# Performance work log

Measured on AMD Instinct MI355X. Metric: run time of the kernel, lower is better.

Reference implementation:

```python
import jax, jax.numpy as jnp
import numpy as np

C = 512
QK = C // 8  # 64
B, L = 8, 4096


def setup_inputs() -> dict:
    key = jax.random.key(0)
    ks = jax.random.split(key, 8)
    s = 0.02
    return {
        "x": jax.random.normal(ks[0], (B, C, L), dtype=jnp.float32),
        "Wq": jax.random.normal(ks[1], (QK, C), dtype=jnp.float32) * s,
        "bq": jax.random.normal(ks[2], (QK,), dtype=jnp.float32) * s,
        "Wk": jax.random.normal(ks[3], (QK, C), dtype=jnp.float32) * s,
        "bk": jax.random.normal(ks[4], (QK,), dtype=jnp.float32) * s,
        "Wv": jax.random.normal(ks[5], (C, C), dtype=jnp.float32) * s,
        "bv": jax.random.normal(ks[6], (C,), dtype=jnp.float32) * s,
        "gamma": jax.random.normal(ks[7], (1,), dtype=jnp.float32) * 0.1,
    }


def reference(x, Wq, bq, Wk, bk, Wv, bv, gamma):
    # 1x1 convs are per-position linear projections over channels
    q = jnp.einsum('bcl,dc->bld', x, Wq) + bq            # [B, L, QK]  (proj_query, permuted)
    k = jnp.einsum('bcl,dc->bdl', x, Wk) + bk[:, None]   # [B, QK, L]  (proj_key)
    v = jnp.einsum('bcl,dc->bdl', x, Wv) + bv[:, None]   # [B, C, L]   (proj_value)
    energy = jnp.einsum('bid,bdj->bij', q, k)            # [B, L, L]
    attn = jax.nn.softmax(energy, axis=-1)               # softmax over j
    out = jnp.einsum('bcj,bij->bci', v, attn)            # [B, C, L]
    return gamma * out + x
```

## Files before the change

kernel.cpp:

```cpp
#include <hip/hip_runtime.h>
#include <math.h>

#define BB 8
#define CC 512
#define LL 4096
#define DQK 64

typedef short short8 __attribute__((ext_vector_type(8)));
typedef unsigned short ushort4v __attribute__((ext_vector_type(4)));
typedef unsigned short ushort8v __attribute__((ext_vector_type(8)));
typedef float floatx4 __attribute__((ext_vector_type(4)));
typedef unsigned int uint4v __attribute__((ext_vector_type(4)));

__device__ __forceinline__ unsigned short f2bf(float f) {
    union { float f; unsigned u; } v; v.f = f;
    unsigned r = v.u + 0x7fffu + ((v.u >> 16) & 1u);
    return (unsigned short)(r >> 16);
}

__device__ __forceinline__ void load_lds16(const void* gptr, void* lptr) {
    __builtin_amdgcn_global_load_lds(
        (const __attribute__((address_space(1))) unsigned int*)gptr,
        (__attribute__((address_space(3))) unsigned int*)lptr, 16, 0, 0);
}

__device__ __forceinline__ unsigned cvt_pk_bf16(float lo, float hi) {
    unsigned r;
    asm("v_cvt_pk_bf16_f32 %0, %1, %2" : "=v"(r) : "v"(lo), "v"(hi));
    return r;
}

__global__ __launch_bounds__(256) void k_transpose(const float* __restrict__ x,
                                                   unsigned short* __restrict__ xt) {
    __shared__ unsigned short tile[64][72];
    int l0 = blockIdx.x * 64, c0 = blockIdx.y * 64, b = blockIdx.z;
    int t = threadIdx.x;
    int r  = t >> 2;
    int ch = (t & 3) * 16;
    const float* src = x + ((size_t)b * CC + c0 + r) * LL + l0 + ch;
#pragma unroll
    for (int j = 0; j < 4; ++j) {
        floatx4 v = *(const floatx4*)(src + j * 4);
        ushort4v u = { f2bf(v[0]), f2bf(v[1]), f2bf(v[2]), f2bf(v[3]) };
        *(ushort4v*)(&tile[r][ch + j * 4]) = u;
    }
    __syncthreads();
    int lr  = t >> 2;
    int cch = (t & 3) * 16;
    ushort8v o0, o1;
#pragma unroll
    for (int j = 0; j < 8; ++j) o0[j] = tile[cch + j][lr];
#pragma unroll
    for (int j = 0; j < 8; ++j) o1[j] = tile[cch + 8 + j][lr];
    unsigned short* dst = xt + ((size_t)b * LL + l0 + lr) * CC + c0 + cch;
    *(ushort8v*)(dst)     = o0;
    *(ushort8v*)(dst + 8) = o1;
}

__global__ void k_castw(const float* __restrict__ wq, const float* __restrict__ wk,
                        const float* __restrict__ wv,
                        unsigned short* __restrict__ wqb, unsigned short* __restrict__ wkb,
                        unsigned short* __restrict__ wvb) {
    int i = blockIdx.x * 256 + threadIdx.x;
    if (i < DQK * CC) { wqb[i] = f2bf(wq[i]); wkb[i] = f2bf(wk[i]); }
    wvb[i] = f2bf(wv[i]);
}

__global__ __launch_bounds__(256) void k_proj(const unsigned short* __restrict__ xt,
                                              const unsigned short* __restrict__ wb,
                                              const float* __restrict__ bias,
                                              unsigned short* __restrict__ out,
                                              float scale) {
    int l0 = blockIdx.x * 64;
    int b  = blockIdx.y;
    int tid = threadIdx.x;
    int w = tid >> 6, lane = tid & 63;
    int lane16 = lane & 15, g = lane >> 4;
    __shared__ unsigned short wtile[64 * 512];
    {
        int pg = tid & 63;
#pragma unroll
        for (int ci = 0; ci < 16; ++ci) {
            int r  = ci * 4 + (tid >> 6);
            int sg = (pg & 56) | ((pg ^ r) & 7);
            load_lds16(wb + (size_t)r * CC + sg * 8, wtile + ((size_t)ci * 256 + tid) * 8);
        }
    }
    const unsigned short* xrow = xt + ((size_t)b * LL + l0 + w * 16 + lane16) * CC + g * 8;
    short8 afrag[16];
#pragma unroll
    for (int kk = 0; kk < 16; ++kk) afrag[kk] = *(const short8*)(xrow + kk * 32);
    __syncthreads();

    int xe = (g ^ (lane16 & 7)) * 8;
    int xo = ((g + 4) ^ (lane16 & 7)) * 8;
#pragma unroll
    for (int nt = 0; nt < 4; ++nt) {
        int dl = nt * 16 + lane16;
        floatx4 acc = {0.f, 0.f, 0.f, 0.f};
#pragma unroll
        for (int kk = 0; kk < 16; ++kk) {
            int off = dl * 512 + (kk >> 1) * 64 + ((kk & 1) ? xo : xe);
            short8 bfrag = *(const short8*)(wtile + off);
            acc = __builtin_amdgcn_mfma_f32_16x16x32_bf16(afrag[kk], bfrag, acc, 0, 0, 0);
        }
        float bv = bias[dl];
#pragma unroll
        for (int r = 0; r < 4; ++r) {
            int lidx = l0 + w * 16 + g * 4 + r;
            out[((size_t)b * LL + lidx) * DQK + dl] = f2bf((acc[r] + bv) * scale);
        }
    }
}

__global__ __launch_bounds__(256) void k_projT(const unsigned short* __restrict__ xt,
                                               const unsigned short* __restrict__ wb,
                                               const float* __restrict__ bias,
                                               unsigned short* __restrict__ out) {
    int l0 = blockIdx.x * 64;
    int b  = blockIdx.y;
    int tid = threadIdx.x;
    int w = tid >> 6, lane = tid & 63;
    int lane16 = lane & 15, g = lane >> 4;
    __shared__ unsigned short xtile[64 * 512];
    {
        const unsigned short* xg = xt + ((size_t)b * LL + l0) * CC;
        int pg = tid & 63;
#pragma unroll
        for (int ci = 0; ci < 16; ++ci) {
            int r  = ci * 4 + (tid >> 6);
            int sg = (pg & 56) | ((pg ^ r) & 7);
            load_lds16(xg + (size_t)r * CC + sg * 8, xtile + ((size_t)ci * 256 + tid) * 8);
        }
    }
    __syncthreads();

    int xe = (g ^ (lane16 & 7)) * 8;
    int xo = ((g + 4) ^ (lane16 & 7)) * 8;
    for (int z = 0; z < 8; ++z) {
        int dw = z * 64 + w * 16;
        const unsigned short* wrow = wb + (size_t)(dw + lane16) * CC + g * 8;
        short8 afrag[16];
#pragma unroll
        for (int kk = 0; kk < 16; ++kk) afrag[kk] = *(const short8*)(wrow + kk * 32);
#pragma unroll
        for (int nt = 0; nt < 4; ++nt) {
            floatx4 acc = {0.f, 0.f, 0.f, 0.f};
#pragma unroll
            for (int kk = 0; kk < 16; ++kk) {
                int off = (nt * 16 + lane16) * 512 + (kk >> 1) * 64 + ((kk & 1) ? xo : xe);
                short8 bfrag = *(const short8*)(xtile + off);
                acc = __builtin_amdgcn_mfma_f32_16x16x32_bf16(afrag[kk], bfrag, acc, 0, 0, 0);
            }
            int l = l0 + nt * 16 + lane16;
#pragma unroll
            for (int r = 0; r < 4; ++r) {
                int d = dw + g * 4 + r;
                out[((size_t)b * CC + d) * LL + l] = f2bf(acc[r] + bias[d]);
            }
        }
    }
}

__global__ __launch_bounds__(256, 2) void k_attn(const unsigned short* __restrict__ q,
                                                 const unsigned short* __restrict__ kws,
                                                 const unsigned short* __restrict__ vws,
                                                 const float* __restrict__ x,
                                                 const float* __restrict__ gamma,
                                                 float* __restrict__ out) {
    int i0 = blockIdx.x * 128;
    int b  = blockIdx.y;
    int c0 = blockIdx.z * 256;
    int tid = threadIdx.x;
    int w = tid >> 6, lane = tid & 63;
    int lane16 = lane & 15, g = lane >> 4;
    int iw = i0 + w * 32;

    __shared__ unsigned short kt[2][64 * 64];
    __shared__ unsigned short vt[2][256 * 64];

    short8 qf[2][2];
#pragma unroll
    for (int m = 0; m < 2; ++m) {
        const unsigned short* qrow = q + ((size_t)b * LL + iw + m * 16 + lane16) * DQK + g * 8;
        qf[m][0] = *(const short8*)(qrow);
        qf[m][1] = *(const short8*)(qrow + 32);
    }

    const unsigned short* kglob = kws + (size_t)b * LL * DQK;
    const unsigned short* vglob = vws + ((size_t)b * CC + c0) * LL;
    int gr    = (tid & 7) ^ ((tid >> 3) & 7);
    int koff0 = (tid >> 3) * DQK + gr * 8;
    int voff0 = (tid >> 3) * LL  + gr * 8;

    int kro[2], vro[2];
#pragma unroll
    for (int kk = 0; kk < 2; ++kk) {
        int sw = (kk * 4 + g) ^ (lane16 & 7);
        kro[kk] = lane16 * 64 + sw * 8;
        vro[kk] = lane16 * 64 + sw * 8;
    }

    short8 ones;
#pragma unroll
    for (int j = 0; j < 8; ++j) ones[j] = (short)0x3f80;

    floatx4 O[2][16];
#pragma unroll
    for (int m = 0; m < 2; ++m)
#pragma unroll
        for (int nt = 0; nt < 16; ++nt) O[m][nt] = {0.f, 0.f, 0.f, 0.f};
    floatx4 Ol[2];
#pragma unroll
    for (int m = 0; m < 2; ++m) Ol[m] = {0.f, 0.f, 0.f, 0.f};

    auto stage = [&](int j0n, int buf) {
        const unsigned short* ks = kglob + j0n * DQK + koff0;
        unsigned short* kd = &kt[buf][tid * 8];
        load_lds16(ks, kd);
        load_lds16(ks + 2048, kd + 2048);
        const unsigned short* vs = vglob + j0n + voff0;
        unsigned short* vd = &vt[buf][tid * 8];
#pragma unroll
        for (int i = 0; i < 8; ++i)
            load_lds16(vs + i * 131072, vd + i * 2048);
    };

    stage(0, 0);
    int cur = 0;
    for (int j0 = 0; j0 < LL; j0 += 64) {
        __syncthreads();
        if (j0 + 64 < LL) stage(j0 + 64, cur ^ 1);

        const unsigned short* kb = kt[cur];
        const unsigned short* vb = vt[cur];

        floatx4 S[2][4];
#pragma unroll
        for (int m = 0; m < 2; ++m)
#pragma unroll
            for (int nt = 0; nt < 4; ++nt) S[m][nt] = {0.f, 0.f, 0.f, 0.f};
#pragma unroll
        for (int nt = 0; nt < 4; ++nt) {
            short8 k0 = *(const short8*)(kb + kro[0] + nt * 1024);
#pragma unroll
            for (int m = 0; m < 2; ++m)
                S[m][nt] = __builtin_amdgcn_mfma_f32_16x16x32_bf16(k0, qf[m][0], S[m][nt], 0, 0, 0);
        }
#pragma unroll
        for (int nt = 0; nt < 4; ++nt) {
            short8 k1 = *(const short8*)(kb + kro[1] + nt * 1024);
#pragma unroll
            for (int m = 0; m < 2; ++m)
                S[m][nt] = __builtin_amdgcn_mfma_f32_16x16x32_bf16(k1, qf[m][1], S[m][nt], 0, 0, 0);
        }

        short8 pa[2][2];
#pragma unroll
        for (int m = 0; m < 2; ++m) {
#pragma unroll
            for (int kk = 0; kk < 2; ++kk) {
                floatx4 p0, p1;
#pragma unroll
                for (int r = 0; r < 4; ++r) {
                    p0[r] = __builtin_amdgcn_exp2f(S[m][2 * kk][r]);
                    p1[r] = __builtin_amdgcn_exp2f(S[m][2 * kk + 1][r]);
                }
                unsigned A0 = cvt_pk_bf16(p0[0], p0[1]);
                unsigned A1 = cvt_pk_bf16(p0[2], p0[3]);
                unsigned B0 = cvt_pk_bf16(p1[0], p1[1]);
                unsigned B1 = cvt_pk_bf16(p1[2], p1[3]);
                asm("v_permlane32_swap_b32 %0, %1" : "+v"(A0), "+v"(B0));
                asm("v_permlane16_swap_b32 %0, %1" : "+v"(A0), "+v"(B0));
                asm("v_permlane32_swap_b32 %0, %1" : "+v"(A1), "+v"(B1));
                asm("v_permlane16_swap_b32 %0, %1" : "+v"(A1), "+v"(B1));
                uint4v pw = { A0, A1, B0, B1 };
                pa[m][kk] = *(short8*)&pw;
            }
#pragma unroll
            for (int kk = 0; kk < 2; ++kk)
                Ol[m] = __builtin_amdgcn_mfma_f32_16x16x32_bf16(pa[m][kk], ones, Ol[m], 0, 0, 0);
        }

        __builtin_amdgcn_s_setprio(1);
#pragma unroll
        for (int kk = 0; kk < 2; ++kk)
#pragma unroll
            for (int nt = 0; nt < 16; ++nt) {
                short8 vf = *(const short8*)(vb + vro[kk] + nt * 1024);
#pragma unroll
                for (int m = 0; m < 2; ++m)
                    O[m][nt] = __builtin_amdgcn_mfma_f32_16x16x32_bf16(pa[m][kk], vf, O[m][nt], 0, 0, 0);
            }
        __builtin_amdgcn_s_setprio(0);
        cur ^= 1;
    }

    float linv[2][4];
#pragma unroll
    for (int m = 0; m < 2; ++m)
#pragma unroll
        for (int r = 0; r < 4; ++r) linv[m][r] = 1.f / Ol[m][r];

    float gam = gamma[0];
#pragma unroll
    for (int m = 0; m < 2; ++m)
#pragma unroll
        for (int nt = 0; nt < 16; ++nt) {
            int c = c0 + nt * 16 + lane16;
            size_t base = ((size_t)b * CC + c) * LL + iw + m * 16 + g * 4;
            floatx4 xv = *(const floatx4*)(x + base);
            floatx4 o;
#pragma unroll
            for (int r = 0; r < 4; ++r) o[r] = gam * (O[m][nt][r] * linv[m][r]) + xv[r];
            *(floatx4*)(out + base) = o;
        }
}

extern "C" void kernel_launch(void* const* d_in, const int* in_sizes, int n_in,
                              void* d_out, int out_size, void* d_ws, size_t ws_size,
                              hipStream_t stream) {
    const float* x     = (const float*)d_in[0];
    const float* Wq    = (const float*)d_in[1];
    const float* bq    = (const float*)d_in[2];
    const float* Wk    = (const float*)d_in[3];
    const float* bk    = (const float*)d_in[4];
    const float* Wv    = (const float*)d_in[5];
    const float* bv    = (const float*)d_in[6];
    const float* gamma = (const float*)d_in[7];
    float* out = (float*)d_out;

    unsigned short* xt  = (unsigned short*)d_ws;
    unsigned short* qb  = xt  + (size_t)BB * LL * CC;
    unsigned short* kb  = qb  + (size_t)BB * LL * DQK;
    unsigned short* vb  = kb  + (size_t)BB * LL * DQK;
    unsigned short* wqb = vb  + (size_t)BB * CC * LL;
    unsigned short* wkb = wqb + (size_t)DQK * CC;
    unsigned short* wvb = wkb + (size_t)DQK * CC;

    const float LOG2E = 1.4426950408889634f;
    k_transpose<<<dim3(LL / 64, CC / 64, BB), 256, 0, stream>>>(x, xt);
    k_castw<<<dim3((CC * CC) / 256), 256, 0, stream>>>(Wq, Wk, Wv, wqb, wkb, wvb);
    k_proj<<<dim3(LL / 64, BB), 256, 0, stream>>>(xt, wqb, bq, qb, LOG2E);
    k_proj<<<dim3(LL / 64, BB), 256, 0, stream>>>(xt, wkb, bk, kb, 1.0f);
    k_projT<<<dim3(LL / 64, BB), 256, 0, stream>>>(xt, wvb, bv, vb);
    k_attn<<<dim3(LL / 128, BB, CC / 256), 256, 0, stream>>>(qb, kb, vb, x, gamma, out);
}
```

Before: 376.8 us.

## Fuse Q/K/V projections into one kernel, remap attention blocks, split softmax to overlap MFMA

Merges the three projection kernels into one k_projall that loads each x tile into LDS once and computes V, Q and K from it, double-buffering the weight fragments in registers. Q/K outputs are written as 4-element vectors. The attention kernel gets a swizzled block-to-tile mapping, likely meant to group blocks sharing K/V for cache locality. Its inner loop splits exp/softmax into two halves so the PV MFMAs on the first half can overlap the exponentials of the second. This adds register pressure from the doubled weight fragments and reorders MFMA accumulation.

```diff
diff --git a/kernel.cpp b/kernel.cpp
--- a/kernel.cpp
+++ b/kernel.cpp
@@ -66,57 +66,16 @@
     wvb[i] = f2bf(wv[i]);
 }
 
-__global__ __launch_bounds__(256) void k_proj(const unsigned short* __restrict__ xt,
-                                              const unsigned short* __restrict__ wb,
-                                              const float* __restrict__ bias,
-                                              unsigned short* __restrict__ out,
-                                              float scale) {
-    int l0 = blockIdx.x * 64;
-    int b  = blockIdx.y;
-    int tid = threadIdx.x;
-    int w = tid >> 6, lane = tid & 63;
-    int lane16 = lane & 15, g = lane >> 4;
-    __shared__ unsigned short wtile[64 * 512];
-    {
-        int pg = tid & 63;
-#pragma unroll
-        for (int ci = 0; ci < 16; ++ci) {
-            int r  = ci * 4 + (tid >> 6);
-            int sg = (pg & 56) | ((pg ^ r) & 7);
-            load_lds16(wb + (size_t)r * CC + sg * 8, wtile + ((size_t)ci * 256 + tid) * 8);
-        }
-    }
-    const unsigned short* xrow = xt + ((size_t)b * LL + l0 + w * 16 + lane16) * CC + g * 8;
-    short8 afrag[16];
-#pragma unroll
-    for (int kk = 0; kk < 16; ++kk) afrag[kk] = *(const short8*)(xrow + kk * 32);
-    __syncthreads();
-
-    int xe = (g ^ (lane16 & 7)) * 8;
-    int xo = ((g + 4) ^ (lane16 & 7)) * 8;
-#pragma unroll
-    for (int nt = 0; nt < 4; ++nt) {
-        int dl = nt * 16 + lane16;
-        floatx4 acc = {0.f, 0.f, 0.f, 0.f};
-#pragma unroll
-        for (int kk = 0; kk < 16; ++kk) {
-            int off = dl * 512 + (kk >> 1) * 64 + ((kk & 1) ? xo : xe);
-            short8 bfrag = *(const short8*)(wtile + off);
-            acc = __builtin_amdgcn_mfma_f32_16x16x32_bf16(afrag[kk], bfrag, acc, 0, 0, 0);
-        }
-        float bv = bias[dl];
-#pragma unroll
-        for (int r = 0; r < 4; ++r) {
-            int lidx = l0 + w * 16 + g * 4 + r;
-            out[((size_t)b * LL + lidx) * DQK + dl] = f2bf((acc[r] + bv) * scale);
-        }
-    }
-}
-
-__global__ __launch_bounds__(256) void k_projT(const unsigned short* __restrict__ xt,
-                                               const unsigned short* __restrict__ wb,
-                                               const float* __restrict__ bias,
-                                               unsigned short* __restrict__ out) {
+__global__ __launch_bounds__(256) void k_projall(const unsigned short* __restrict__ xt,
+                                                 const unsigned short* __restrict__ wqb,
+                                                 const unsigned short* __restrict__ wkb,
+                                                 const unsigned short* __restrict__ wvb,
+                                                 const float* __restrict__ bq,
+                                                 const float* __restrict__ bk,
+                                                 const float* __restrict__ bv,
+                                                 unsigned short* __restrict__ qout,
+                                                 unsigned short* __restrict__ kout,
+                                                 unsigned short* __restrict__ vout) {
     int l0 = blockIdx.x * 64;
     int b  = blockIdx.y;
     int tid = threadIdx.x;
@@ -133,16 +92,21 @@
             load_lds16(xg + (size_t)r * CC + sg * 8, xtile + ((size_t)ci * 256 + tid) * 8);
         }
     }
-    __syncthreads();
 
     int xe = (g ^ (lane16 & 7)) * 8;
     int xo = ((g + 4) ^ (lane16 & 7)) * 8;
-    for (int z = 0; z < 8; ++z) {
-        int dw = z * 64 + w * 16;
-        const unsigned short* wrow = wb + (size_t)(dw + lane16) * CC + g * 8;
-        short8 afrag[16];
-#pragma unroll
-        for (int kk = 0; kk < 16; ++kk) afrag[kk] = *(const short8*)(wrow + kk * 32);
+
+    auto loadW = [&](short8 (&af)[16], int z) {
+        const unsigned short* base;
+        if (z < 8)       base = wvb + (size_t)(z * 64 + w * 16 + lane16) * CC;
+        else if (z == 8) base = wqb + (size_t)(w * 16 + lane16) * CC;
+        else             base = wkb + (size_t)(w * 16 + lane16) * CC;
+        base += g * 8;
+#pragma unroll
+        for (int kk = 0; kk < 16; ++kk) af[kk] = *(const short8*)(base + kk * 32);
+    };
+
+    auto comp = [&](short8 (&af)[16], int z) {
 #pragma unroll
         for (int nt = 0; nt < 4; ++nt) {
             floatx4 acc = {0.f, 0.f, 0.f, 0.f};
@@ -150,15 +114,38 @@
             for (int kk = 0; kk < 16; ++kk) {
                 int off = (nt * 16 + lane16) * 512 + (kk >> 1) * 64 + ((kk & 1) ? xo : xe);
                 short8 bfrag = *(const short8*)(xtile + off);
-                acc = __builtin_amdgcn_mfma_f32_16x16x32_bf16(afrag[kk], bfrag, acc, 0, 0, 0);
+                acc = __builtin_amdgcn_mfma_f32_16x16x32_bf16(af[kk], bfrag, acc, 0, 0, 0);
             }
             int l = l0 + nt * 16 + lane16;
-#pragma unroll
-            for (int r = 0; r < 4; ++r) {
-                int d = dw + g * 4 + r;
-                out[((size_t)b * CC + d) * LL + l] = f2bf(acc[r] + bias[d]);
+            if (z < 8) {
+#pragma unroll
+                for (int r = 0; r < 4; ++r) {
+                    int d = z * 64 + w * 16 + g * 4 + r;
+                    vout[((size_t)b * CC + d) * LL + l] = f2bf(acc[r] + bv[d]);
+                }
+            } else {
+                const float* bias = (z == 8) ? bq : bk;
+                float sc = (z == 8) ? 1.4426950408889634f : 1.0f;
+                ushort4v o;
+#pragma unroll
+                for (int r = 0; r < 4; ++r)
+                    o[r] = f2bf((acc[r] + bias[w * 16 + g * 4 + r]) * sc);
+                unsigned short* dst = ((z == 8) ? qout : kout)
+                                      + ((size_t)b * LL + l) * DQK + w * 16 + g * 4;
+                *(ushort4v*)dst = o;
             }
         }
+    };
+
+    short8 afA[16], afB[16];
+    loadW(afA, 0);
+    __syncthreads();
+
+    for (int z = 0; z < 10; z += 2) {
+        loadW(afB, z + 1);
+        comp(afA, z);
+        if (z + 2 < 10) loadW(afA, z + 2);
+        comp(afB, z + 1);
     }
 }
 
@@ -168,9 +155,14 @@
                                                  const float* __restrict__ x,
                                                  const float* __restrict__ gamma,
                                                  float* __restrict__ out) {
-    int i0 = blockIdx.x * 128;
-    int b  = blockIdx.y;
-    int c0 = blockIdx.z * 256;
+    int bid = blockIdx.x + 32 * blockIdx.y + 256 * blockIdx.z;
+    int x8  = bid & 7;
+    int ii  = bid >> 3;
+    int wg  = (x8 + 8 * (ii >> 5)) * 32 + (ii & 31);
+    int i0 = (wg & 31) * 128;
+    int b  = (wg >> 5) & 7;
+    int c0 = (wg >> 8) * 256;
+
     int tid = threadIdx.x;
     int w = tid >> 6, lane = tid & 63;
     int lane16 = lane & 15, g = lane >> 4;
@@ -226,72 +218,97 @@
             load_lds16(vs + i * 131072, vd + i * 2048);
     };
 
+    auto softmax_half = [&](floatx4 (&Sh)[2][2], short8 (&paD)[2]) {
+#pragma unroll
+        for (int m = 0; m < 2; ++m) {
+            float e0[4], e1[4];
+#pragma unroll
+            for (int r = 0; r < 4; ++r) {
+                e0[r] = __builtin_amdgcn_exp2f(Sh[m][0][r]);
+                e1[r] = __builtin_amdgcn_exp2f(Sh[m][1][r]);
+            }
+            unsigned A0 = cvt_pk_bf16(e0[0], e0[1]);
+            unsigned A1 = cvt_pk_bf16(e0[2], e0[3]);
+            unsigned B0 = cvt_pk_bf16(e1[0], e1[1]);
+            unsigned B1 = cvt_pk_bf16(e1[2], e1[3]);
+            asm("v_permlane32_swap_b32 %0, %1" : "+v"(A0), "+v"(B0));
+            asm("v_permlane16_swap_b32 %0, %1" : "+v"(A0), "+v"(B0));
+            asm("v_permlane32_swap_b32 %0, %1" : "+v"(A1), "+v"(B1));
+            asm("v_permlane16_swap_b32 %0, %1" : "+v"(A1), "+v"(B1));
+            uint4v pw = { A0, A1, B0, B1 };
+            paD[m] = *(short8*)&pw;
+            Ol[m] = __builtin_amdgcn_mfma_f32_16x16x32_bf16(paD[m], ones, Ol[m], 0, 0, 0);
+        }
+    };
+
     stage(0, 0);
     int cur = 0;
     for (int j0 = 0; j0 < LL; j0 += 64) {
         __syncthreads();
         if (j0 + 64 < LL) stage(j0 + 64, cur ^ 1);
 
-        const unsigned short* kb = kt[cur];
-        const unsigned short* vb = vt[cur];
-
-        floatx4 S[2][4];
+        const unsigned short* kbp = kt[cur];
+        const unsigned short* vbp = vt[cur];
+
+        floatx4 Sa[2][2], Sb[2][2];
 #pragma unroll
         for (int m = 0; m < 2; ++m)
 #pragma unroll
-            for (int nt = 0; nt < 4; ++nt) S[m][nt] = {0.f, 0.f, 0.f, 0.f};
-#pragma unroll
-        for (int nt = 0; nt < 4; ++nt) {
-            short8 k0 = *(const short8*)(kb + kro[0] + nt * 1024);
+            for (int nt = 0; nt < 2; ++nt) { Sa[m][nt] = {0.f,0.f,0.f,0.f}; Sb[m][nt] = {0.f,0.f,0.f,0.f}; }
+
+        short8 ka0 = *(const short8*)(kbp + kro[0]);
+        short8 ka1 = *(const short8*)(kbp + kro[1]);
+        short8 kb0 = *(const short8*)(kbp + kro[0] + 1024);
+        short8 kb1 = *(const short8*)(kbp + kro[1] + 1024);
+#pragma unroll
+        for (int m = 0; m < 2; ++m) {
+            Sa[m][0] = __builtin_amdgcn_mfma_f32_16x16x32_bf16(ka0, qf[m][0], Sa[m][0], 0, 0, 0);
+            Sa[m][0] = __builtin_amdgcn_mfma_f32_16x16x32_bf16(ka1, qf[m][1], Sa[m][0], 0, 0, 0);
+            Sa[m][1] = __builtin_amdgcn_mfma_f32_16x16x32_bf16(kb0, qf[m][0], Sa[m][1], 0, 0, 0);
+            Sa[m][1] = __builtin_amdgcn_mfma_f32_16x16x32_bf16(kb1, qf[m][1], Sa[m][1], 0, 0, 0);
+        }
+        short8 kc0 = *(const short8*)(kbp + kro[0] + 2048);
+        short8 kc1 = *(const short8*)(kbp + kro[1] + 2048);
+        short8 kd0 = *(const short8*)(kbp + kro[0] + 3072);
+        short8 kd1 = *(const short8*)(kbp + kro[1] + 3072);
+#pragma unroll
+        for (int m = 0; m < 2; ++m) {
+            Sb[m][0] = __builtin_amdgcn_mfma_f32_16x16x32_bf16(kc0, qf[m][0], Sb[m][0], 0, 0, 0);
+            Sb[m][0] = __builtin_amdgcn_mfma_f32_16x16x32_bf16(kc1, qf[m][1], Sb[m][0], 0, 0, 0);
+            Sb[m][1] = __builtin_amdgcn_mfma_f32_16x16x32_bf16(kd0, qf[m][0], Sb[m][1], 0, 0, 0);
+            Sb[m][1] = __builtin_amdgcn_mfma_f32_16x16x32_bf16(kd1, qf[m][1], Sb[m][1], 0, 0, 0);
+        }
+
+        short8 pa0[2], pa1[2];
+        softmax_half(Sa, pa0);
+
+        __builtin_amdgcn_s_setprio(1);
+#pragma unroll
+        for (int nt = 0; nt < 8; ++nt) {
+            short8 vf = *(const short8*)(vbp + vro[0] + nt * 1024);
 #pragma unroll
             for (int m = 0; m < 2; ++m)
-                S[m][nt] = __builtin_amdgcn_mfma_f32_16x16x32_bf16(k0, qf[m][0], S[m][nt], 0, 0, 0);
-        }
-#pragma unroll
-        for (int nt = 0; nt < 4; ++nt) {
-            short8 k1 = *(const short8*)(kb + kro[1] + nt * 1024);
+                O[m][nt] = __builtin_amdgcn_mfma_f32_16x16x32_bf16(pa0[m], vf, O[m][nt], 0, 0, 0);
+        }
+        __builtin_amdgcn_s_setprio(0);
+
+        softmax_half(Sb, pa1);
+
+        __builtin_amdgcn_s_setprio(1);
+#pragma unroll
+        for (int nt = 8; nt < 16; ++nt) {
+            short8 vf = *(const short8*)(vbp + vro[0] + nt * 1024);
 #pragma unroll
             for (int m = 0; m < 2; ++m)
-                S[m][nt] = __builtin_amdgcn_mfma_f32_16x16x32_bf16(k1, qf[m][1], S[m][nt], 0, 0, 0);
-        }
-
-        short8 pa[2][2];
-#pragma unroll
-        for (int m = 0; m < 2; ++m) {
-#pragma unroll
-            for (int kk = 0; kk < 2; ++kk) {
-                floatx4 p0, p1;
-#pragma unroll
-                for (int r = 0; r < 4; ++r) {
-                    p0[r] = __builtin_amdgcn_exp2f(S[m][2 * kk][r]);
-                    p1[r] = __builtin_amdgcn_exp2f(S[m][2 * kk + 1][r]);
-                }
-                unsigned A0 = cvt_pk_bf16(p0[0], p0[1]);
-                unsigned A1 = cvt_pk_bf16(p0[2], p0[3]);
-                unsigned B0 = cvt_pk_bf16(p1[0], p1[1]);
-                unsigned B1 = cvt_pk_bf16(p1[2], p1[3]);
-                asm("v_permlane32_swap_b32 %0, %1" : "+v"(A0), "+v"(B0));
-                asm("v_permlane16_swap_b32 %0, %1" : "+v"(A0), "+v"(B0));
-                asm("v_permlane32_swap_b32 %0, %1" : "+v"(A1), "+v"(B1));
-                asm("v_permlane16_swap_b32 %0, %1" : "+v"(A1), "+v"(B1));
-                uint4v pw = { A0, A1, B0, B1 };
-                pa[m][kk] = *(short8*)&pw;
-            }
-#pragma unroll
-            for (int kk = 0; kk < 2; ++kk)
-                Ol[m] = __builtin_amdgcn_mfma_f32_16x16x32_bf16(pa[m][kk], ones, Ol[m], 0, 0, 0);
-        }
-
-        __builtin_amdgcn_s_setprio(1);
-#pragma unroll
-        for (int kk = 0; kk < 2; ++kk)
-#pragma unroll
-            for (int nt = 0; nt < 16; ++nt) {
-                short8 vf = *(const short8*)(vb + vro[kk] + nt * 1024);
-#pragma unroll
-                for (int m = 0; m < 2; ++m)
-                    O[m][nt] = __builtin_amdgcn_mfma_f32_16x16x32_bf16(pa[m][kk], vf, O[m][nt], 0, 0, 0);
-            }
+                O[m][nt] = __builtin_amdgcn_mfma_f32_16x16x32_bf16(pa0[m], vf, O[m][nt], 0, 0, 0);
+        }
+#pragma unroll
+        for (int nt = 0; nt < 16; ++nt) {
+            short8 vf = *(const short8*)(vbp + vro[1] + nt * 1024);
+#pragma unroll
+            for (int m = 0; m < 2; ++m)
+                O[m][nt] = __builtin_amdgcn_mfma_f32_16x16x32_bf16(pa1[m], vf, O[m][nt], 0, 0, 0);
+        }
         __builtin_amdgcn_s_setprio(0);
         cur ^= 1;
     }
@@ -338,11 +355,8 @@
     unsigned short* wkb = wqb + (size_t)DQK * CC;
     unsigned short* wvb = wkb + (size_t)DQK * CC;
 
-    const float LOG2E = 1.4426950408889634f;
     k_transpose<<<dim3(LL / 64, CC / 64, BB), 256, 0, stream>>>(x, xt);
     k_castw<<<dim3((CC * CC) / 256), 256, 0, stream>>>(Wq, Wk, Wv, wqb, wkb, wvb);
-    k_proj<<<dim3(LL / 64, BB), 256, 0, stream>>>(xt, wqb, bq, qb, LOG2E);
-    k_proj<<<dim3(LL / 64, BB), 256, 0, stream>>>(xt, wkb, bk, kb, 1.0f);
-    k_projT<<<dim3(LL / 64, BB), 256, 0, stream>>>(xt, wvb, bv, vb);
+    k_projall<<<dim3(LL / 64, BB), 256, 0, stream>>>(xt, wqb, wkb, wvb, bq, bk, bv, qb, kb, vb);
     k_attn<<<dim3(LL / 128, BB, CC / 256), 256, 0, stream>>>(qb, kb, vb, x, gamma, out);
 }
```

After: 356.5 us. 1.06x faster.
